# Kernel tuning notes

Hardware: AMD Instinct MI355X
Metric: run time of the kernel (lower is better)

Reference implementation:

```python
import jax, jax.numpy as jnp
import numpy as np

N = 50000      # num nodes
C_IN = 128     # channels[0]
C_OUT = 128    # channels[1]
D = 16         # fixed node degree
T = 4          # diffusion steps
H_MLP = 64     # diff_mlp hidden
H_GRU = 128    # GRUAggr hidden
EPS = 0.01


def setup_inputs() -> dict:
    key = jax.random.key(0)
    ks = jax.random.split(key, 10)
    node_attr = jax.random.normal(ks[0], (N, C_IN), jnp.float32)
    # adjacency sorted by source: node i owns columns [i*D, i*D+D)
    src = jnp.repeat(jnp.arange(N), D)
    dst = jax.random.randint(ks[1], (N * D,), 0, N)
    edge_index = jnp.stack([src, dst])                       # [2, N*D]
    slices = jnp.stack([jnp.arange(N) * D, jnp.full((N,), D)], axis=1)  # [N,2] (start,count)
    noise = EPS * jax.random.normal(ks[2], (T, N, D), jnp.float32)      # eps*randn per step
    init = lambda k, shape, fan: (jax.random.normal(k, shape, jnp.float32) / np.sqrt(fan))
    W1 = init(ks[3], ((1 + T) * C_IN, H_MLP), (1 + T) * C_IN)
    b1 = jnp.zeros((H_MLP,), jnp.float32)
    W2 = init(ks[4], (H_MLP, 1), H_MLP)
    b2 = jnp.zeros((1,), jnp.float32)
    Wx = init(ks[5], (C_IN, 3 * H_GRU), C_IN)
    Wh = init(ks[6], (H_GRU, 3 * H_GRU), H_GRU)
    bx = jnp.zeros((3 * H_GRU,), jnp.float32)
    bh = jnp.zeros((3 * H_GRU,), jnp.float32)
    Wo = init(ks[7], (H_GRU, C_OUT), H_GRU)
    bo = jnp.zeros((C_OUT,), jnp.float32)
    return dict(node_attr=node_attr, edge_index=edge_index, slices=slices, noise=noise,
                W1=W1, b1=b1, W2=W2, b2=b2, Wx=Wx, Wh=Wh, bx=bx, bh=bh, Wo=Wo, bo=bo)


def _gru(x_seq, Wx, Wh, bx, bh):
    # x_seq: [T+1, N, C]; torch GRU gate order (r, z, n)
    H = Wh.shape[0]
    def step(h, x):
        gx = x @ Wx + bx
        gh = h @ Wh + bh
        xr, xz, xn = jnp.split(gx, 3, axis=-1)
        hr, hz, hn = jnp.split(gh, 3, axis=-1)
        r = jax.nn.sigmoid(xr + hr)
        z = jax.nn.sigmoid(xz + hz)
        n = jnp.tanh(xn + r * hn)
        return (1.0 - z) * n + z * h, None
    h0 = jnp.zeros((x_seq.shape[1], H), x_seq.dtype)
    h, _ = jax.lax.scan(step, h0, x_seq)
    return h


def reference(node_attr, edge_index, slices, noise, W1, b1, W2, b2, Wx, Wh, bx, bh, Wo, bo):
    n, C = node_attr.shape
    t_steps, _, deg = noise.shape
    dst = edge_index[1]
    walk_embeds = jnp.zeros((n, 1 + t_steps, C), node_attr.dtype).at[:, 0, :].set(node_attr)
    cur = jnp.arange(n)
    for t in range(t_steps):
        starts = slices[cur, 0]                              # slice_cat(adj, adj_slic_t)
        nbr = dst[starts[:, None] + jnp.arange(deg)]         # [N, D] neighbor node ids
        v_t = node_attr[nbr]                                 # [N, D, C]
        # diff_mlp on [prefix walk embed | candidate neighbor]: split the first
        # linear layer so the shared prefix is computed once per node (position
        # 1+t of walk_embeds is still zero, matching the original fill order).
        h_pre = walk_embeds.reshape(n, (1 + t_steps) * C) @ W1 + b1       # [N, H_MLP]
        h_nbr = jnp.einsum('ndc,ch->ndh', v_t, W1[(1 + t) * C:(2 + t) * C])
        logp = (jax.nn.relu(h_pre[:, None, :] + h_nbr) @ W2)[..., 0] + b2[0]  # [N, D]
        logp = jax.lax.stop_gradient(logp)                   # torch.no_grad()
        # scatter_logsumexp over init node == logsumexp over the D candidates
        p = jnp.exp(logp - jax.nn.logsumexp(logp, axis=1, keepdims=True)) + noise[t]
        sel = jnp.argmax(p, axis=1)                          # scatter_max per init node
        cur = nbr[jnp.arange(n), sel]                        # walks_t
        walk_embeds = walk_embeds.at[:, 1 + t, :].set(node_attr[cur])
    h = _gru(jnp.transpose(walk_embeds, (1, 0, 2)), Wx, Wh, bx, bh)
    return h @ Wo + bo                                       # [N, C_OUT]
```

## Files before the change

### kernel.cpp

```cpp
#include <hip/hip_runtime.h>
#include <math.h>

#define NND 50000
#define DEG 16

typedef __attribute__((ext_vector_type(8))) short short8v;
typedef __attribute__((ext_vector_type(4))) float float4v;

#define OFF_HPRE 0ULL
#define OFF_PROJ 12800000ULL
#define OFF_XB   64000000ULL
#define OFF_IDX  102400000ULL
#define OFF_BQF  103600384ULL
#define OFF_WOF  103862528ULL
#define WS_NEED  103895296ULL

#define LOG2E 1.44269504088896f

__device__ __forceinline__ float fast_sig(float x){
    return __builtin_amdgcn_rcpf(1.f + __builtin_amdgcn_exp2f(-LOG2E*x));
}
__device__ __forceinline__ float fast_tanh(float x){
    return fmaf(-2.f, __builtin_amdgcn_rcpf(1.f + __builtin_amdgcn_exp2f((2.f*LOG2E)*x)), 1.f);
}
__device__ __forceinline__ unsigned short f2bf(float f){
    unsigned int u = __float_as_uint(f);
    u += 0x7FFFu + ((u >> 16) & 1u);
    return (unsigned short)(u >> 16);
}
__device__ __forceinline__ float bf2f(unsigned short h){
    return __uint_as_float(((unsigned int)h) << 16);
}

__global__ __launch_bounds__(256) void k_setup(const float* __restrict__ na,
    const float* __restrict__ Wx, const float* __restrict__ Wh,
    const float* __restrict__ Wo, unsigned short* __restrict__ Xb,
    unsigned short* __restrict__ BqF, unsigned short* __restrict__ WoF,
    int* __restrict__ idx0)
{
    const int b = blockIdx.x, tid = threadIdx.x;
    {
        int i = b*256 + tid;
        if (i < NND*32){
            float4 v = *(const float4*)(na + (size_t)i*4);
            unsigned long long pk = (unsigned long long)f2bf(v.x)
                | ((unsigned long long)f2bf(v.y) << 16)
                | ((unsigned long long)f2bf(v.z) << 32)
                | ((unsigned long long)f2bf(v.w) << 48);
            *(unsigned long long*)(Xb + (size_t)i*4) = pk;
        }
    }
    if (b < 512){
        int i = b*256 + tid;
        int jj = i & 7, lane = (i>>3)&63, ct = (i>>9)&7, c = (i>>12)&7, y = i>>15;
        int g = ct>>1, jh = ct&1, mm = lane&15, quad = lane>>4;
        int jg = (y<<5) + (jh<<4) + mm;
        int k = (c<<5) + (quad<<3) + jj;
        float v = 0.f;
        if (k < 128){
            if (g < 3) v = Wh[k*384 + g*128 + jg];
        } else {
            int kk = k - 128;
            if (g == 0)      v = Wx[kk*384 + jg];
            else if (g == 1) v = Wx[kk*384 + 128 + jg];
            else if (g == 3) v = Wx[kk*384 + 256 + jg];
        }
        BqF[i] = f2bf(v);
    } else if (b < 576){
        int i = (b-512)*256 + tid;
        int jj = i & 7, lane = (i>>3)&63, ct = (i>>9)&7, c = i>>12;
        int n = (ct<<4) + (lane&15);
        int k = (c<<5) + ((lane>>4)<<3) + jj;
        WoF[i] = f2bf(Wo[k*128 + n]);
    } else if (b < 772){
        int i = (b-576)*256 + tid;
        if (i < NND) idx0[i] = i;
    }
}

__global__ __launch_bounds__(256,2) void k_projall(const float* __restrict__ A,
    const float* __restrict__ W1, const float* __restrict__ bias1,
    float* __restrict__ hpre, float* __restrict__ proj)
{
    __shared__ float Alt[32][320];
    __shared__ float Bl[32][140];
    const int tid = threadIdx.x;
    const int row0 = blockIdx.x << 8;
    const int z = blockIdx.y;
    const int row_t = tid >> 4, col_t = tid & 15;
    const int sr_st = tid + ((tid>>4)<<2);
    int gr_st = row0 + tid; if (gr_st >= NND) gr_st = NND-1;
    const float* ap = A + (size_t)gr_st*128;

    if (z < 2){
        float4 acc[16][2];
#pragma unroll
        for (int j=0;j<16;j++){ acc[j][0]=make_float4(0,0,0,0); acc[j][1]=make_float4(0,0,0,0); }
        const int cb = col_t << 3;
        const int scb = cb + ((cb>>5)<<2);
        for (int k0 = 0; k0 < 128; k0 += 32){
#pragma unroll
            for (int u=0;u<8;u++){
                float4 v = *(const float4*)(ap + k0 + (u<<2));
                Alt[(u<<2)+0][sr_st] = v.x; Alt[(u<<2)+1][sr_st] = v.y;
                Alt[(u<<2)+2][sr_st] = v.z; Alt[(u<<2)+3][sr_st] = v.w;
            }
#pragma unroll
            for (int i=0;i<4;i++){
                int p = (i<<8) + tid;
                int ch = p >> 9, rem = p & 511;
                int bk = rem >> 4, bc = (rem & 15) << 2;
                int col = (ch<<6) + bc;
                int sc = col + ((col>>5)<<2);
                *(float4*)(&Bl[bk][sc]) =
                    *(const float4*)(W1 + (size_t)(((z*2+ch)<<7) + k0 + bk)*64 + bc);
            }
            __syncthreads();
#pragma unroll 2
            for (int k=0;k<32;k++){
                const float* ar = &Alt[k][row_t*20];
                float4 a0 = *(const float4*)(ar);
                float4 a1 = *(const float4*)(ar+4);
                float4 a2 = *(const float4*)(ar+8);
                float4 a3 = *(const float4*)(ar+12);
                float4 b0 = *(const float4*)(&Bl[k][scb]);
                float4 b1 = *(const float4*)(&Bl[k][scb+4]);
                float av[16] = {a0.x,a0.y,a0.z,a0.w, a1.x,a1.y,a1.z,a1.w,
                                a2.x,a2.y,a2.z,a2.w, a3.x,a3.y,a3.z,a3.w};
#pragma unroll
                for (int j=0;j<16;j++){
                    acc[j][0].x = fmaf(av[j], b0.x, acc[j][0].x);
                    acc[j][0].y = fmaf(av[j], b0.y, acc[j][0].y);
                    acc[j][0].z = fmaf(av[j], b0.z, acc[j][0].z);
                    acc[j][0].w = fmaf(av[j], b0.w, acc[j][0].w);
                    acc[j][1].x = fmaf(av[j], b1.x, acc[j][1].x);
                    acc[j][1].y = fmaf(av[j], b1.y, acc[j][1].y);
                    acc[j][1].z = fmaf(av[j], b1.z, acc[j][1].z);
                    acc[j][1].w = fmaf(av[j], b1.w, acc[j][1].w);
                }
            }
            __syncthreads();
        }
        float* dlo = (z==0) ? hpre : (proj + (size_t)(2*z-1)*NND*64);
        float* dhi = proj + (size_t)(2*z)*NND*64;
        float* dstp = (col_t < 8) ? dlo : dhi;
        const int ccol = (col_t & 7) << 3;
        float4 bb0 = make_float4(0,0,0,0), bb1 = make_float4(0,0,0,0);
        if (z == 0 && col_t < 8){
            bb0 = *(const float4*)(bias1 + ccol);
            bb1 = *(const float4*)(bias1 + ccol + 4);
        }
#pragma unroll
        for (int j=0;j<16;j++){
            int gr = row0 + (row_t<<4) + j;
            if (gr < NND){
                float4 o0 = make_float4(acc[j][0].x+bb0.x, acc[j][0].y+bb0.y,
                                        acc[j][0].z+bb0.z, acc[j][0].w+bb0.w);
                float4 o1 = make_float4(acc[j][1].x+bb1.x, acc[j][1].y+bb1.y,
                                        acc[j][1].z+bb1.z, acc[j][1].w+bb1.w);
                *(float4*)(dstp + ((size_t)gr<<6) + ccol)     = o0;
                *(float4*)(dstp + ((size_t)gr<<6) + ccol + 4) = o1;
            }
        }
    } else {
        float4 acc[16];
#pragma unroll
        for (int j=0;j<16;j++) acc[j] = make_float4(0,0,0,0);
        const int cb = col_t << 2;
        const int scb = cb + ((cb>>5)<<2);
        for (int k0 = 0; k0 < 128; k0 += 32){
#pragma unroll
            for (int u=0;u<8;u++){
                float4 v = *(const float4*)(ap + k0 + (u<<2));
                Alt[(u<<2)+0][sr_st] = v.x; Alt[(u<<2)+1][sr_st] = v.y;
                Alt[(u<<2)+2][sr_st] = v.z; Alt[(u<<2)+3][sr_st] = v.w;
            }
#pragma unroll
            for (int i=0;i<2;i++){
                int p = (i<<8) + tid;
                int bk = p >> 4, bc = (p & 15) << 2;
                int sc = bc + ((bc>>5)<<2);
                *(float4*)(&Bl[bk][sc]) =
                    *(const float4*)(W1 + (size_t)((4<<7) + k0 + bk)*64 + bc);
            }
            __syncthreads();
#pragma unroll 2
            for (int k=0;k<32;k++){
                const float* ar = &Alt[k][row_t*20];
                float4 a0 = *(const float4*)(ar);
                float4 a1 = *(const float4*)(ar+4);
                float4 a2 = *(const float4*)(ar+8);
                float4 a3 = *(const float4*)(ar+12);
                float4 b0 = *(const float4*)(&Bl[k][scb]);
                float av[16] = {a0.x,a0.y,a0.z,a0.w, a1.x,a1.y,a1.z,a1.w,
                                a2.x,a2.y,a2.z,a2.w, a3.x,a3.y,a3.z,a3.w};
#pragma unroll
                for (int j=0;j<16;j++){
                    acc[j].x = fmaf(av[j], b0.x, acc[j].x);
                    acc[j].y = fmaf(av[j], b0.y, acc[j].y);
                    acc[j].z = fmaf(av[j], b0.z, acc[j].z);
                    acc[j].w = fmaf(av[j], b0.w, acc[j].w);
                }
            }
            __syncthreads();
        }
        float* dstp = proj + (size_t)3*NND*64;
#pragma unroll
        for (int j=0;j<16;j++){
            int gr = row0 + (row_t<<4) + j;
            if (gr < NND)
                *(float4*)(dstp + ((size_t)gr<<6) + cb) = acc[j];
        }
    }
}

__global__ __launch_bounds__(256) void k_walk4(
    const float* __restrict__ hpre0, const float* __restrict__ proj,
    const int* __restrict__ dst, const float* __restrict__ W2,
    const float* __restrict__ b2, const float* __restrict__ noise,
    int* __restrict__ idxb)
{
    const int tid = threadIdx.x;
    const int sg = tid >> 4, l = tid & 15;
    const int gi = (blockIdx.x << 4) + sg;
    float4 hp = *(const float4*)(hpre0 + ((size_t)gi<<6) + (l<<2));
    float4 w2 = *(const float4*)(W2 + (l<<2));
    const float b2s = b2[0];
    int curv = gi;
#pragma unroll 1
    for (int t=0; t<4; t++){
        const float* pj = proj + (size_t)t*NND*64;
        const int base = curv*DEG;
        const int nbr = dst[base + l];
        int4 nb0 = *(const int4*)(dst + base);
        int4 nb1 = *(const int4*)(dst + base + 4);
        int4 nb2 = *(const int4*)(dst + base + 8);
        int4 nb3 = *(const int4*)(dst + base + 12);
        int nds[16] = {nb0.x,nb0.y,nb0.z,nb0.w, nb1.x,nb1.y,nb1.z,nb1.w,
                       nb2.x,nb2.y,nb2.z,nb2.w, nb3.x,nb3.y,nb3.z,nb3.w};
        float4 val[16];
#pragma unroll
        for (int d=0; d<16; d++)
            val[d] = *(const float4*)(pj + ((size_t)nds[d]<<6) + (l<<2));
        float q[16];
#pragma unroll
        for (int d=0; d<16; d++){
            float4 v = val[d];
            float qq =  fmaxf(hp.x+v.x,0.f)*w2.x;
            qq = fmaf(fmaxf(hp.y+v.y,0.f), w2.y, qq);
            qq = fmaf(fmaxf(hp.z+v.z,0.f), w2.z, qq);
            qq = fmaf(fmaxf(hp.w+v.w,0.f), w2.w, qq);
            q[d] = qq;
        }
        float r1[8];
#pragma unroll
        for (int i=0;i<8;i++){
            float a = q[2*i], b = q[2*i+1];
            float send = (l&1) ? a : b;
            float keep = (l&1) ? b : a;
            r1[i] = keep + __shfl_xor(send, 1, 16);
        }
        float r2[4];
#pragma unroll
        for (int i=0;i<4;i++){
            float a = r1[2*i], b = r1[2*i+1];
            float send = (l&2) ? a : b;
            float keep = (l&2) ? b : a;
            r2[i] = keep + __shfl_xor(send, 2, 16);
        }
        float r3[2];
#pragma unroll
        for (int i=0;i<2;i++){
            float a = r2[2*i], b = r2[2*i+1];
            float send = (l&4) ? a : b;
            float keep = (l&4) ? b : a;
            r3[i] = keep + __shfl_xor(send, 4, 16);
        }
        float lp;
        {
            float a = r3[0], b = r3[1];
            float send = (l&8) ? a : b;
            float keep = (l&8) ? b : a;
            lp = keep + __shfl_xor(send, 8, 16) + b2s;
        }
        float mx = lp;
#pragma unroll
        for (int off=8; off; off>>=1) mx = fmaxf(mx, __shfl_xor(mx, off, 16));
        float s = expf(lp - mx);
#pragma unroll
        for (int off=8; off; off>>=1) s += __shfl_xor(s, off, 16);
        float p = expf(lp - mx - logf(s)) + noise[(size_t)t*NND*DEG + ((size_t)gi<<4) + l];
        float bv = p; int bi = l;
#pragma unroll
        for (int off=8; off; off>>=1){
            float ov = __shfl_xor(bv, off, 16);
            int   oi = __shfl_xor(bi, off, 16);
            if (ov > bv || (ov == bv && oi < bi)){ bv = ov; bi = oi; }
        }
        int sel = __shfl(nbr, bi, 16);
        if (l == 0) idxb[(size_t)(t+1)*NND + gi] = sel;
        float4 u = *(const float4*)(pj + ((size_t)sel<<6) + (l<<2));
        hp.x += u.x; hp.y += u.y; hp.z += u.z; hp.w += u.w;
        curv = sel;
    }
}

__global__ __launch_bounds__(256,2) void k_gru5(
    const unsigned short* __restrict__ Xb,
    const unsigned short* __restrict__ BqF,
    const unsigned short* __restrict__ WoF,
    const float* __restrict__ bx, const float* __restrict__ bh,
    const float* __restrict__ bo, const int* __restrict__ idxb,
    float* __restrict__ out)
{
    __shared__ unsigned short A_l[2][8192];
    __shared__ unsigned short X_l[16384];
    const int tid = threadIdx.x;
    const int w = tid >> 6, lane = tid & 63;
    const int m = lane & 15, quad = lane >> 4;
    const int r = tid & 63, q = tid >> 6;
    const int rt_s = r >> 4, m_s = r & 15;
    float brr[2], bzz[2], bxn[2], bhn[2];
#pragma unroll
    for (int jh=0; jh<2; jh++){
        int j = (w<<5) + (jh<<4) + m;
        brr[jh] = bx[j] + bh[j];
        bzz[jh] = bx[128+j] + bh[128+j];
        bxn[jh] = bx[256+j];
        bhn[jh] = bh[256+j];
    }

#pragma unroll 1
    for (int tb = blockIdx.x; tb < 782; tb += 512){
        const int row0 = tb << 6;
        int gr = row0 + r; if (gr >= NND) gr = NND-1;
        unsigned short holdv[2][4][4];
        short8v xv[4];
        {
            const int xr = idxb[gr];
            const unsigned short* xrow = Xb + (size_t)xr*128 + (q<<5);
#pragma unroll
            for (int u=0;u<4;u++) xv[u] = *(const short8v*)(xrow + (u<<3));
#pragma unroll
            for (int u=0;u<4;u++)
                *(short8v*)(X_l + (((rt_s<<2)+q)*64 + (u<<4) + m_s)*8) = xv[u];
            const int xr1 = idxb[NND + gr];
            const unsigned short* xrow1 = Xb + (size_t)xr1*128 + (q<<5);
#pragma unroll
            for (int u=0;u<4;u++) xv[u] = *(const short8v*)(xrow1 + (u<<3));
        }
        __syncthreads();

#pragma unroll 1
        for (int s=0; s<5; s++){
            const unsigned short* Acur = A_l[s&1];
            const unsigned short* Xcur = X_l + ((s&1)<<13);
            if (s < 4){
                unsigned short* Xnxt = X_l + (((s+1)&1)<<13);
#pragma unroll
                for (int u=0;u<4;u++)
                    *(short8v*)(Xnxt + (((rt_s<<2)+q)*64 + (u<<4) + m_s)*8) = xv[u];
                if (s < 3){
                    const int xr = idxb[(size_t)(s+2)*NND + gr];
                    const unsigned short* xrow = Xb + (size_t)xr*128 + (q<<5);
#pragma unroll
                    for (int u=0;u<4;u++) xv[u] = *(const short8v*)(xrow + (u<<3));
                }
            }
            float4v zero = {0.f,0.f,0.f,0.f};
            float4v acc[32];
#pragma unroll
            for (int i=0;i<32;i++) acc[i] = zero;
            if (s > 0){
#pragma unroll 1
                for (int c=0;c<4;c++){
                    short8v afr[4];
#pragma unroll
                    for (int rt=0;rt<4;rt++)
                        afr[rt] = *(const short8v*)(Acur + (((rt<<2) + c)*64 + lane)*8);
                    const unsigned short* bp = BqF + ((((size_t)w*8 + c)*8)*64 + lane)*8;
#pragma unroll
                    for (int ct=0;ct<6;ct++){
                        short8v bf = *(const short8v*)(bp + (ct<<9));
#pragma unroll
                        for (int rt=0;rt<4;rt++)
                            acc[(ct<<2)+rt] = __builtin_amdgcn_mfma_f32_16x16x32_bf16(afr[rt], bf, acc[(ct<<2)+rt], 0,0,0);
                    }
                }
            }
#pragma unroll 1
            for (int c=4;c<8;c++){
                short8v afr[4];
#pragma unroll
                for (int rt=0;rt<4;rt++)
                    afr[rt] = *(const short8v*)(Xcur + (((rt<<2) + (c&3))*64 + lane)*8);
                const unsigned short* bp = BqF + ((((size_t)w*8 + c)*8)*64 + lane)*8;
#pragma unroll
                for (int cti=0;cti<6;cti++){
                    const int ct = (cti < 4) ? cti : (cti + 2);
                    short8v bf = *(const short8v*)(bp + (ct<<9));
#pragma unroll
                    for (int rt=0;rt<4;rt++)
                        acc[(ct<<2)+rt] = __builtin_amdgcn_mfma_f32_16x16x32_bf16(afr[rt], bf, acc[(ct<<2)+rt], 0,0,0);
                }
            }
#pragma unroll
            for (int jh=0; jh<2; jh++){
#pragma unroll
                for (int rt=0; rt<4; rt++){
#pragma unroll
                    for (int r4=0; r4<4; r4++){
                        float rg = fast_sig(acc[(jh<<2)+rt][r4] + brr[jh]);
                        float zg = fast_sig(acc[((2+jh)<<2)+rt][r4] + bzz[jh]);
                        float ng = fast_tanh(acc[((6+jh)<<2)+rt][r4] + bxn[jh] + rg*(acc[((4+jh)<<2)+rt][r4] + bhn[jh]));
                        float hold = (s == 0) ? 0.f : bf2f(holdv[jh][rt][r4]);
                        holdv[jh][rt][r4] = f2bf((1.f - zg)*ng + zg*hold);
                    }
                }
            }
            unsigned short* Anxt = A_l[(s+1)&1];
#pragma unroll
            for (int jh=0; jh<2; jh++)
#pragma unroll
                for (int rt=0; rt<4; rt++)
#pragma unroll
                    for (int r4=0; r4<4; r4++){
                        int ha = ((((rt<<2)+w)*64 + (((jh<<1)+(m>>3))<<4) + (quad<<2)+r4)<<3) + (m&7);
                        Anxt[ha] = holdv[jh][rt][r4];
                    }
            __syncthreads();
        }
        const unsigned short* Afin = A_l[1];
        float4v zero = {0.f,0.f,0.f,0.f};
        float4v acco[8];
#pragma unroll
        for (int i=0;i<8;i++) acco[i] = zero;
#pragma unroll 1
        for (int c=0;c<4;c++){
            short8v afr[4];
#pragma unroll
            for (int rt=0;rt<4;rt++)
                afr[rt] = *(const short8v*)(Afin + (((rt<<2) + c)*64 + lane)*8);
#pragma unroll
            for (int cto=0;cto<2;cto++){
                short8v bf = *(const short8v*)(WoF + (((size_t)(c*8 + (w<<1)+cto))*64 + lane)*8);
#pragma unroll
                for (int rt=0;rt<4;rt++)
                    acco[(cto<<2)+rt] = __builtin_amdgcn_mfma_f32_16x16x32_bf16(afr[rt], bf, acco[(cto<<2)+rt], 0,0,0);
            }
        }
#pragma unroll
        for (int cto=0; cto<2; cto++){
            int col = (w<<5) + (cto<<4) + m;
            float bb = bo[col];
#pragma unroll
            for (int rt=0; rt<4; rt++){
#pragma unroll
                for (int r4=0; r4<4; r4++){
                    int row = row0 + (rt<<4) + (quad<<2) + r4;
                    if (row < NND) out[(size_t)row*128 + col] = acco[(cto<<2)+rt][r4] + bb;
                }
            }
        }
    }
}

extern "C" void kernel_launch(void* const* d_in, const int* in_sizes, int n_in,
                              void* d_out, int out_size, void* d_ws, size_t ws_size,
                              hipStream_t stream)
{
    const float* node_attr = (const float*)d_in[0];
    const int*   edge_index= (const int*)  d_in[1];
    const float* noise = (const float*)d_in[3];
    const float* W1 = (const float*)d_in[4];
    const float* b1 = (const float*)d_in[5];
    const float* W2 = (const float*)d_in[6];
    const float* b2 = (const float*)d_in[7];
    const float* Wx = (const float*)d_in[8];
    const float* Wh = (const float*)d_in[9];
    const float* bx = (const float*)d_in[10];
    const float* bh = (const float*)d_in[11];
    const float* Wo = (const float*)d_in[12];
    const float* bo = (const float*)d_in[13];
    const int* dst = edge_index + (size_t)NND*DEG;
    float* out = (float*)d_out;
    if (ws_size < WS_NEED) return;

    char* ws = (char*)d_ws;
    float* hpre = (float*)(ws + OFF_HPRE);
    float* proj = (float*)(ws + OFF_PROJ);
    unsigned short* Xb  = (unsigned short*)(ws + OFF_XB);
    int* idxb = (int*)(ws + OFF_IDX);
    unsigned short* BqF = (unsigned short*)(ws + OFF_BQF);
    unsigned short* WoF = (unsigned short*)(ws + OFF_WOF);

    k_setup<<<dim3(6250), dim3(256), 0, stream>>>(node_attr, Wx, Wh, Wo, Xb, BqF, WoF, idxb);

    k_projall<<<dim3(196, 3), dim3(256), 0, stream>>>(node_attr, W1, b1, hpre, proj);
    k_walk4<<<dim3(3125), dim3(256), 0, stream>>>(hpre, proj, dst, W2, b2, noise, idxb);

    k_gru5<<<dim3(512), dim3(256), 0, stream>>>(Xb, BqF, WoF, bx, bh, bo, idxb, out);
}
```

Before: 348.6 us.

## Split GRU gate accumulation by column half and single-buffer hidden state for occupancy

The GRU kernel now computes the gate accumulators in two passes over the hidden-column halves (jh), keeping 16 accumulators live instead of 32. This cuts register pressure so launch bounds can be raised to 3 blocks per CU. The hidden-state LDS buffer is single-buffered, with an extra barrier before it is overwritten, and the grid grows to 768 blocks. The cost is re-reading the A/X fragments once per half and one more __syncthreads per step.

After: 425.6 us. +22.1%, slower.

```diff
diff --git a/kernel.cpp b/kernel.cpp
--- a/kernel.cpp
+++ b/kernel.cpp
@@ -305,7 +305,7 @@
     }
 }
 
-__global__ __launch_bounds__(256,2) void k_gru5(
+__global__ __launch_bounds__(256,3) void k_gru5(
     const unsigned short* __restrict__ Xb,
     const unsigned short* __restrict__ BqF,
     const unsigned short* __restrict__ WoF,
@@ -313,7 +313,7 @@
     const float* __restrict__ bo, const int* __restrict__ idxb,
     float* __restrict__ out)
 {
-    __shared__ unsigned short A_l[2][8192];
+    __shared__ unsigned short A_l[8192];
     __shared__ unsigned short X_l[16384];
     const int tid = threadIdx.x;
     const int w = tid >> 6, lane = tid & 63;
@@ -331,7 +331,7 @@
     }
 
 #pragma unroll 1
-    for (int tb = blockIdx.x; tb < 782; tb += 512){
+    for (int tb = blockIdx.x; tb < 782; tb += 768){
         const int row0 = tb << 6;
         int gr = row0 + r; if (gr >= NND) gr = NND-1;
         unsigned short holdv[2][4][4];
@@ -353,7 +353,6 @@
 
 #pragma unroll 1
         for (int s=0; s<5; s++){
-            const unsigned short* Acur = A_l[s&1];
             const unsigned short* Xcur = X_l + ((s&1)<<13);
             if (s < 4){
                 unsigned short* Xnxt = X_l + (((s+1)&1)<<13);
@@ -367,58 +366,60 @@
                     for (int u=0;u<4;u++) xv[u] = *(const short8v*)(xrow + (u<<3));
                 }
             }
-            float4v zero = {0.f,0.f,0.f,0.f};
-            float4v acc[32];
-#pragma unroll
-            for (int i=0;i<32;i++) acc[i] = zero;
-            if (s > 0){
-#pragma unroll 1
-                for (int c=0;c<4;c++){
+#pragma unroll 1
+            for (int jh=0; jh<2; jh++){
+                float4v zero = {0.f,0.f,0.f,0.f};
+                float4v acc[16];
+#pragma unroll
+                for (int i=0;i<16;i++) acc[i] = zero;
+                if (s > 0){
+#pragma unroll 1
+                    for (int c=0;c<4;c++){
+                        short8v afr[4];
+#pragma unroll
+                        for (int rt=0;rt<4;rt++)
+                            afr[rt] = *(const short8v*)(A_l + (((rt<<2) + c)*64 + lane)*8);
+                        const unsigned short* bp = BqF + ((((size_t)w*8 + c)*8)*64 + lane)*8;
+#pragma unroll
+                        for (int g=0;g<3;g++){
+                            const int ct = (g<<1) + jh;
+                            short8v bf = *(const short8v*)(bp + (ct<<9));
+#pragma unroll
+                            for (int rt=0;rt<4;rt++)
+                                acc[(g<<2)+rt] = __builtin_amdgcn_mfma_f32_16x16x32_bf16(afr[rt], bf, acc[(g<<2)+rt], 0,0,0);
+                        }
+                    }
+                }
+#pragma unroll 1
+                for (int c=4;c<8;c++){
                     short8v afr[4];
 #pragma unroll
                     for (int rt=0;rt<4;rt++)
-                        afr[rt] = *(const short8v*)(Acur + (((rt<<2) + c)*64 + lane)*8);
+                        afr[rt] = *(const short8v*)(Xcur + (((rt<<2) + (c&3))*64 + lane)*8);
                     const unsigned short* bp = BqF + ((((size_t)w*8 + c)*8)*64 + lane)*8;
 #pragma unroll
-                    for (int ct=0;ct<6;ct++){
+                    for (int gi2=0;gi2<3;gi2++){
+                        const int g = (gi2 < 2) ? gi2 : 3;
+                        const int ct = (g<<1) + jh;
                         short8v bf = *(const short8v*)(bp + (ct<<9));
 #pragma unroll
                         for (int rt=0;rt<4;rt++)
-                            acc[(ct<<2)+rt] = __builtin_amdgcn_mfma_f32_16x16x32_bf16(afr[rt], bf, acc[(ct<<2)+rt], 0,0,0);
+                            acc[(g<<2)+rt] = __builtin_amdgcn_mfma_f32_16x16x32_bf16(afr[rt], bf, acc[(g<<2)+rt], 0,0,0);
                     }
                 }
-            }
-#pragma unroll 1
-            for (int c=4;c<8;c++){
-                short8v afr[4];
-#pragma unroll
-                for (int rt=0;rt<4;rt++)
-                    afr[rt] = *(const short8v*)(Xcur + (((rt<<2) + (c&3))*64 + lane)*8);
-                const unsigned short* bp = BqF + ((((size_t)w*8 + c)*8)*64 + lane)*8;
-#pragma unroll
-                for (int cti=0;cti<6;cti++){
-                    const int ct = (cti < 4) ? cti : (cti + 2);
-                    short8v bf = *(const short8v*)(bp + (ct<<9));
-#pragma unroll
-                    for (int rt=0;rt<4;rt++)
-                        acc[(ct<<2)+rt] = __builtin_amdgcn_mfma_f32_16x16x32_bf16(afr[rt], bf, acc[(ct<<2)+rt], 0,0,0);
-                }
-            }
-#pragma unroll
-            for (int jh=0; jh<2; jh++){
 #pragma unroll
                 for (int rt=0; rt<4; rt++){
 #pragma unroll
                     for (int r4=0; r4<4; r4++){
-                        float rg = fast_sig(acc[(jh<<2)+rt][r4] + brr[jh]);
-                        float zg = fast_sig(acc[((2+jh)<<2)+rt][r4] + bzz[jh]);
-                        float ng = fast_tanh(acc[((6+jh)<<2)+rt][r4] + bxn[jh] + rg*(acc[((4+jh)<<2)+rt][r4] + bhn[jh]));
+                        float rg = fast_sig(acc[rt][r4] + brr[jh]);
+                        float zg = fast_sig(acc[4+rt][r4] + bzz[jh]);
+                        float ng = fast_tanh(acc[12+rt][r4] + bxn[jh] + rg*(acc[8+rt][r4] + bhn[jh]));
                         float hold = (s == 0) ? 0.f : bf2f(holdv[jh][rt][r4]);
                         holdv[jh][rt][r4] = f2bf((1.f - zg)*ng + zg*hold);
                     }
                 }
             }
-            unsigned short* Anxt = A_l[(s+1)&1];
+            __syncthreads();
 #pragma unroll
             for (int jh=0; jh<2; jh++)
 #pragma unroll
@@ -426,11 +427,10 @@
 #pragma unroll
                     for (int r4=0; r4<4; r4++){
                         int ha = ((((rt<<2)+w)*64 + (((jh<<1)+(m>>3))<<4) + (quad<<2)+r4)<<3) + (m&7);
-                        Anxt[ha] = holdv[jh][rt][r4];
+                        A_l[ha] = holdv[jh][rt][r4];
                     }
             __syncthreads();
         }
-        const unsigned short* Afin = A_l[1];
         float4v zero = {0.f,0.f,0.f,0.f};
         float4v acco[8];
 #pragma unroll
@@ -440,7 +440,7 @@
             short8v afr[4];
 #pragma unroll
             for (int rt=0;rt<4;rt++)
-                afr[rt] = *(const short8v*)(Afin + (((rt<<2) + c)*64 + lane)*8);
+                afr[rt] = *(const short8v*)(A_l + (((rt<<2) + c)*64 + lane)*8);
 #pragma unroll
             for (int cto=0;cto<2;cto++){
                 short8v bf = *(const short8v*)(WoF + (((size_t)(c*8 + (w<<1)+cto))*64 + lane)*8);
@@ -499,5 +499,5 @@
     k_projall<<<dim3(196, 3), dim3(256), 0, stream>>>(node_attr, W1, b1, hpre, proj);
     k_walk4<<<dim3(3125), dim3(256), 0, stream>>>(hpre, proj, dst, W2, b2, noise, idxb);
 
-    k_gru5<<<dim3(512), dim3(256), 0, stream>>>(Xb, BqF, WoF, bx, bh, bo, idxb, out);
-}
+    k_gru5<<<dim3(768), dim3(256), 0, stream>>>(Xb, BqF, WoF, bx, bh, bo, idxb, out);
+}
```
